# Kernel optimization log

Hardware: AMD Instinct MI355X
Metric: run time of the kernel (lower is better)

Reference implementation:

```python
import jax, jax.numpy as jnp
import numpy as np

B, S, D_IN, D_OUT, H = 4, 2048, 1024, 1024, 16
HD = D_OUT // H


def setup_inputs() -> dict:
    key = jax.random.key(0)
    ks = jax.random.split(key, 6)
    s_in = 1.0 / np.sqrt(D_IN)
    s_out = 1.0 / np.sqrt(D_OUT)
    return {
        "x": jax.random.normal(ks[0], (B, S, D_IN), dtype=jnp.float32),
        "W_q": jax.random.uniform(ks[1], (D_OUT, D_IN), jnp.float32, -s_in, s_in),
        "W_k": jax.random.uniform(ks[2], (D_OUT, D_IN), jnp.float32, -s_in, s_in),
        "W_v": jax.random.uniform(ks[3], (D_OUT, D_IN), jnp.float32, -s_in, s_in),
        "W_o": jax.random.uniform(ks[4], (D_OUT, D_OUT), jnp.float32, -s_out, s_out),
        "b_o": jax.random.uniform(ks[5], (D_OUT,), jnp.float32, -s_out, s_out),
    }


def reference(x, W_q, W_k, W_v, W_o, b_o):
    b, s, _ = x.shape
    # torch Linear: y = x @ W.T  (no qkv bias)
    q = (x @ W_q.T).reshape(b, s, H, HD).transpose(0, 2, 1, 3)  # [b,h,s,hd]
    k = (x @ W_k.T).reshape(b, s, H, HD).transpose(0, 2, 1, 3)
    v = (x @ W_v.T).reshape(b, s, H, HD).transpose(0, 2, 1, 3)
    scores = jnp.einsum("bhqd,bhkd->bhqk", q, k)  # [b,h,s,s]
    causal = jnp.triu(jnp.ones((s, s), dtype=bool), k=1)
    scores = jnp.where(causal, -jnp.inf, scores)
    attn = jax.nn.softmax(scores / np.sqrt(HD), axis=-1)
    # dropout p=0.0 -> identity
    ctx = jnp.einsum("bhqk,bhkd->bhqd", attn, v)  # [b,h,s,hd]
    ctx = ctx.transpose(0, 2, 1, 3).reshape(b, s, D_OUT)
    return ctx @ W_o.T + b_o
```

## Files before the change

### kernel.cpp

```cpp
#include <hip/hip_runtime.h>
#include <cstdint>
#include <cstddef>

#define S_LEN  2048
#define NHEAD  16
#define HDIM   64
#define KD     1024
#define BSROWS 8192

typedef __attribute__((ext_vector_type(4))) float          floatx4;
typedef __attribute__((ext_vector_type(8))) __bf16         bf16x8;
typedef __attribute__((ext_vector_type(8))) unsigned short ushort8v;
typedef __attribute__((ext_vector_type(4))) unsigned short ushort4v;
typedef __attribute__((ext_vector_type(4))) float          float4v;

__device__ __forceinline__ unsigned short f2bf(float f) {
  unsigned int u = __float_as_uint(f);
  u += 0x7fffu + ((u >> 16) & 1u);
  return (unsigned short)(u >> 16);
}

#if __has_builtin(__builtin_amdgcn_exp2f)
#define EXP2F(x) __builtin_amdgcn_exp2f(x)
#else
#define EXP2F(x) exp2f(x)
#endif

__device__ __forceinline__ unsigned int pack2bf(float a, float b) {
#if __has_builtin(__builtin_amdgcn_perm)
  return __builtin_amdgcn_perm(__float_as_uint(b), __float_as_uint(a), 0x07060302);
#else
  return (__float_as_uint(a) >> 16) | (__float_as_uint(b) & 0xffff0000u);
#endif
}

__device__ __forceinline__ void async_cp16(const void* gsrc, void* ldst) {
  __builtin_amdgcn_global_load_lds(
      (__attribute__((address_space(1))) void*)gsrc,
      (__attribute__((address_space(3))) void*)ldst,
      16, 0, 0);
}

#define XN4 2097152
#define WN4 262144

__global__ __launch_bounds__(256) void cvt_kernel(
    const float* __restrict__ x,  const float* __restrict__ wq,
    const float* __restrict__ wk, const float* __restrict__ wv,
    const float* __restrict__ wo,
    unsigned short* __restrict__ xb, unsigned short* __restrict__ wqkvb,
    unsigned short* __restrict__ wob)
{
  const int i = blockIdx.x * 256 + threadIdx.x;
  const float* src; unsigned short* dst; int off;
  if (i < XN4) { src = x; dst = xb; off = i; }
  else {
    const int j = i - XN4;
    if (j < WN4)          { src = wq; dst = wqkvb;           off = j; }
    else if (j < 2*WN4)   { src = wk; dst = wqkvb + 4*WN4;   off = j - WN4; }
    else if (j < 3*WN4)   { src = wv; dst = wqkvb + 8*WN4;   off = j - 2*WN4; }
    else                  { src = wo; dst = wob;             off = j - 3*WN4; }
  }
  const float4v v = ((const float4v*)src)[off];
  ushort4v o;
  o.x = f2bf(v.x); o.y = f2bf(v.y); o.z = f2bf(v.z); o.w = f2bf(v.w);
  ((ushort4v*)dst)[off] = o;
}

__global__ __launch_bounds__(256) void gemm_qkv(
    const unsigned short* __restrict__ A,
    const unsigned short* __restrict__ Bw,
    unsigned short* __restrict__ Qo,
    unsigned short* __restrict__ Ko,
    unsigned short* __restrict__ Vto)
{
  __shared__ unsigned short smem[17408];
  const int tid  = threadIdx.x;
  const int wave = tid >> 6, lane = tid & 63;
  const int quad = lane >> 4, l15 = lane & 15;
  const int wr = wave >> 1, wc = wave & 1;
  const int m0 = blockIdx.x * 128, n0 = blockIdx.y * 128;

  const int srow = lane >> 2;
  const int scol = ((lane & 3) ^ ((srow >> 1) & 3)) * 8;
  const unsigned short* gA = A  + (size_t)(m0 + wave * 32 + srow) * KD + scol;
  const unsigned short* gB = Bw + (size_t)(n0 + wave * 32 + srow) * KD + scol;

  const floatx4 fzero = {0.f, 0.f, 0.f, 0.f};
  floatx4 acc[4][4];
#pragma unroll
  for (int i = 0; i < 4; i++)
#pragma unroll
    for (int j = 0; j < 4; j++) acc[i][j] = fzero;

  {
    unsigned short* lA = smem + wave * 1024;
    unsigned short* lB = smem + 4096 + wave * 1024;
    async_cp16(gA,                    lA);
    async_cp16(gA + (size_t)16 * KD,  lA + 512);
    async_cp16(gB,                    lB);
    async_cp16(gB + (size_t)16 * KD,  lB + 512);
  }
  const int lsw = (l15 >> 1) & 3;

#pragma unroll 2
  for (int it = 0; it < 32; it++) {
    asm volatile("s_waitcnt vmcnt(0) lgkmcnt(0)\n\ts_barrier" ::: "memory");
    if (it + 1 < 32) {
      const int nb = (it + 1) & 1;
      const int ko = (it + 1) * 32;
      unsigned short* lA = smem + nb * 8192 + wave * 1024;
      unsigned short* lB = smem + nb * 8192 + 4096 + wave * 1024;
      async_cp16(gA + ko,                   lA);
      async_cp16(gA + ko + (size_t)16 * KD, lA + 512);
      async_cp16(gB + ko,                   lB);
      async_cp16(gB + ko + (size_t)16 * KD, lB + 512);
    }
    const unsigned short* As = smem + (it & 1) * 8192;
    const unsigned short* Bs = As + 4096;

    bf16x8 af[4], bfrag[4];
#pragma unroll
    for (int i = 0; i < 4; i++)
      af[i] = *(const bf16x8*)&As[(wr * 64 + i * 16 + l15) * 32 + (quad ^ lsw) * 8];
#pragma unroll
    for (int j = 0; j < 4; j++)
      bfrag[j] = *(const bf16x8*)&Bs[(wc * 64 + j * 16 + l15) * 32 + (quad ^ lsw) * 8];
#pragma unroll
    for (int i = 0; i < 4; i++)
#pragma unroll
      for (int j = 0; j < 4; j++)
        acc[i][j] = __builtin_amdgcn_mfma_f32_16x16x32_bf16(af[i], bfrag[j], acc[i][j], 0, 0, 0);
  }

  const int which = n0 >> 10;
  const int h0 = (n0 & 1023) >> 6;
  const int b = m0 >> 11, sl = m0 & 2047;

  if (which < 2) {
    unsigned short* dst = which ? Ko : Qo;
    const float scale = which ? 1.0f : 0.18033688011112042f;
    __syncthreads();
    const int crow = wr * 64 + quad * 4;
    const int ccol = wc * 64 + l15;
#pragma unroll
    for (int i = 0; i < 4; i++)
#pragma unroll
      for (int j = 0; j < 4; j++)
#pragma unroll
        for (int r = 0; r < 4; r++)
          smem[(crow + i * 16 + r) * 130 + ccol + j * 16] = f2bf(acc[i][j][r] * scale);
    __syncthreads();
#pragma unroll
    for (int t = 0; t < 8; t++) {
      const int c   = t * 256 + tid;
      const int hd8 = (c & 7) * 8;
      const int hh  = (c >> 3) & 1;
      const int s   = c >> 4;
      const ushort8v val = *(const ushort8v*)&smem[s * 130 + hh * 64 + hd8];
      *(ushort8v*)&dst[((size_t)((b * NHEAD + h0 + hh) * S_LEN + sl + s)) * HDIM + hd8] = val;
    }
  } else {
    __syncthreads();
    const int crow = wr * 64 + quad * 4;
    const int ccol = wc * 64 + l15;
#pragma unroll
    for (int i = 0; i < 4; i++)
#pragma unroll
      for (int j = 0; j < 4; j++) {
        ushort4v t4;
#pragma unroll
        for (int r = 0; r < 4; r++) t4[r] = f2bf(acc[i][j][r]);
        *(ushort4v*)&smem[(ccol + j * 16) * 136 + crow + i * 16] = t4;
      }
    __syncthreads();
#pragma unroll
    for (int t = 0; t < 8; t++) {
      const int c  = t * 256 + tid;
      const int nl = c >> 4, sc = (c & 15) * 8;
      const ushort8v val = *(const ushort8v*)&smem[nl * 136 + sc];
      *(ushort8v*)&Vto[((size_t)((b * NHEAD + h0 + (nl >> 6)) * HDIM + (nl & 63))) * S_LEN + sl + sc] = val;
    }
  }
}

__global__ __launch_bounds__(512, 4) void attn_kernel(
    const unsigned short* __restrict__ Qg_,
    const unsigned short* __restrict__ Kg_,
    const unsigned short* __restrict__ Vtg_,
    unsigned short* __restrict__ CTX)
{
  __shared__ unsigned short smem[33792];
  const int tid  = threadIdx.x, wave = tid >> 6, lane = tid & 63;
  const int quad = lane >> 4, l15 = lane & 15;
  unsigned short* Pw = smem + 16384 + wave * 2176;

  const int bh = (int)blockIdx.x;
  const int yy = (int)blockIdx.y;
  const int qt = (yy < 4) ? yy : (11 - yy);
  const int q0 = qt * 256;
  const size_t base = (size_t)bh * (S_LEN * HDIM);
  const unsigned short* Qg  = Qg_  + base;
  const unsigned short* Kg  = Kg_  + base;
  const unsigned short* Vtg = Vtg_ + base;
  const int qw = q0 + wave * 32;

  const int strow = lane >> 3;
  const int stxc  = (lane & 7) ^ strow;
  const unsigned short* kstage = Kg  + (size_t)(wave * 8 + strow) * HDIM  + stxc * 8;
  const unsigned short* vstage = Vtg + (size_t)(wave * 8 + strow) * S_LEN + stxc * 8;
  unsigned short* kd0 = smem + wave * 512;
  unsigned short* vd0 = smem + 4096 + wave * 512;

  async_cp16(kstage, kd0);
  async_cp16(vstage, vd0);

  bf16x8 qf[2][2];
#pragma unroll
  for (int qtile = 0; qtile < 2; qtile++)
#pragma unroll
    for (int ks = 0; ks < 2; ks++)
      qf[qtile][ks] = *(const bf16x8*)&Qg[(size_t)(qw + qtile * 16 + l15) * HDIM + ks * 32 + quad * 8];

  const int sw0 = ((quad)     ^ (l15 & 7)) * 8;
  const int sw1 = ((4 + quad) ^ (l15 & 7)) * 8;

  const floatx4 fzero = {0.f, 0.f, 0.f, 0.f};
  floatx4 O[2][4];
  float l_part[2] = {0.f, 0.f};
#pragma unroll
  for (int qtile = 0; qtile < 2; qtile++)
#pragma unroll
    for (int mt = 0; mt < 4; mt++) O[qtile][mt] = fzero;

  const int ntiles = 4 * (qt + 1);

  for (int j = 0; j < ntiles; j++) {
    asm volatile("s_waitcnt vmcnt(0) lgkmcnt(0)\n\ts_barrier" ::: "memory");
    if (j + 1 < ntiles) {
      const int nb = (j + 1) & 1;
      async_cp16(kstage + (size_t)(j + 1) * 64 * HDIM, kd0 + nb * 8192);
      async_cp16(vstage + (size_t)(j + 1) * 64,        vd0 + nb * 8192);
    }
    const int k0 = j * 64;
    if (k0 > qw + 31) continue;
    const unsigned short* Ksb = smem + (j & 1) * 8192;
    const unsigned short* Vsb = Ksb + 4096;
    const int krel = qw + 31 - k0;

    bf16x8 kf[4][2];
#pragma unroll
    for (int kt = 0; kt < 4; kt++) {
      if (kt * 16 <= krel) {
        const unsigned short* kr = &Ksb[(kt * 16 + l15) * 64];
        kf[kt][0] = *(const bf16x8*)(kr + sw0);
        kf[kt][1] = *(const bf16x8*)(kr + sw1);
      }
    }

#pragma unroll
    for (int qtile = 0; qtile < 2; qtile++) {
      const int kmax = qw + qtile * 16 + 15;
      if (k0 > kmax) continue;
      floatx4 sa[4];
#pragma unroll
      for (int kt = 0; kt < 4; kt++) sa[kt] = fzero;
#pragma unroll
      for (int kt = 0; kt < 4; kt++) {
        if (k0 + kt * 16 <= kmax) {
          sa[kt] = __builtin_amdgcn_mfma_f32_16x16x32_bf16(kf[kt][0], qf[qtile][0], sa[kt], 0, 0, 0);
          sa[kt] = __builtin_amdgcn_mfma_f32_16x16x32_bf16(kf[kt][1], qf[qtile][1], sa[kt], 0, 0, 0);
        }
      }
      const int qrow = qw + qtile * 16 + l15;
#pragma unroll
      for (int kt = 0; kt < 4; kt++) {
        const int kbase = k0 + kt * 16;
        unsigned short* pdst = &Pw[(qtile * 16 + l15) * 68 + kt * 16 + quad * 4];
        if (kbase <= kmax) {
          if (kbase + 15 > qw + qtile * 16) {
#pragma unroll
            for (int r = 0; r < 4; r++)
              if (kbase + quad * 4 + r > qrow) sa[kt][r] = -INFINITY;
          }
          const float p0 = EXP2F(sa[kt][0]), p1 = EXP2F(sa[kt][1]);
          const float p2 = EXP2F(sa[kt][2]), p3 = EXP2F(sa[kt][3]);
          l_part[qtile] += (p0 + p1) + (p2 + p3);
          uint2 pk; pk.x = pack2bf(p0, p1); pk.y = pack2bf(p2, p3);
          *(uint2*)pdst = pk;
        } else if (k0 + (kt >> 1) * 32 <= kmax) {
          uint2 z; z.x = 0u; z.y = 0u;
          *(uint2*)pdst = z;
        }
      }
    }
    asm volatile("s_waitcnt lgkmcnt(0)" ::: "memory");

#pragma unroll
    for (int ks = 0; ks < 2; ks++) {
      if (ks * 32 > krel) break;
      bf16x8 vf[4];
#pragma unroll
      for (int mt = 0; mt < 4; mt++)
        vf[mt] = *(const bf16x8*)(&Vsb[(mt * 16 + l15) * 64] + (ks ? sw1 : sw0));
#pragma unroll
      for (int qtile = 0; qtile < 2; qtile++) {
        if (k0 + ks * 32 > qw + qtile * 16 + 15) continue;
        const unsigned short* ps = &Pw[(qtile * 16 + l15) * 68 + ks * 32 + quad * 8];
        union { ushort4v h[2]; bf16x8 v; } pu;
        pu.h[0] = *(const ushort4v*)ps;
        pu.h[1] = *(const ushort4v*)(ps + 4);
#pragma unroll
        for (int mt = 0; mt < 4; mt++)
          O[qtile][mt] = __builtin_amdgcn_mfma_f32_16x16x32_bf16(vf[mt], pu.v, O[qtile][mt], 0, 0, 0);
      }
    }
  }

#pragma unroll
  for (int d = 16; d < 64; d <<= 1) {
    l_part[0] += __shfl_xor(l_part[0], d, 64);
    l_part[1] += __shfl_xor(l_part[1], d, 64);
  }

#pragma unroll
  for (int qtile = 0; qtile < 2; qtile++) {
    const float inv = 1.0f / l_part[qtile];
#pragma unroll
    for (int mt = 0; mt < 4; mt++)
#pragma unroll
      for (int a = 0; a < 2; a++) {
        const unsigned int pk =
            (unsigned int)f2bf(O[qtile][mt][2 * a] * inv) |
            ((unsigned int)f2bf(O[qtile][mt][2 * a + 1] * inv) << 16);
        *(unsigned int*)&Pw[(qtile * 16 + l15) * 68 + mt * 16 + quad * 4 + 2 * a] = pk;
      }
  }
  asm volatile("s_waitcnt lgkmcnt(0)" ::: "memory");
  const int b = bh >> 4, h = bh & 15;
#pragma unroll
  for (int it = 0; it < 4; it++) {
    const int g = it * 64 + lane;
    const int row = g >> 3, c8 = (g & 7) * 8;
    union { ushort4v h[2]; ushort8v v; } ou;
    ou.h[0] = *(const ushort4v*)&Pw[row * 68 + c8];
    ou.h[1] = *(const ushort4v*)&Pw[row * 68 + c8 + 4];
    const int s = qw + row;
    *(ushort8v*)&CTX[((size_t)(b * S_LEN + s)) * KD + h * HDIM + c8] = ou.v;
  }
}

__global__ __launch_bounds__(256) void gemm_out(
    const unsigned short* __restrict__ A,
    const unsigned short* __restrict__ Bw,
    const float* __restrict__ bias,
    float* __restrict__ out)
{
  __shared__ unsigned short smem[16384];
  const int tid  = threadIdx.x;
  const int wave = tid >> 6, lane = tid & 63;
  const int quad = lane >> 4, l15 = lane & 15;
  const int wr = wave >> 1, wc = wave & 1;
  const int m0 = blockIdx.x * 128, n0 = blockIdx.y * 128;

  const int srow = lane >> 2;
  const int scol = ((lane & 3) ^ ((srow >> 1) & 3)) * 8;
  const unsigned short* gA = A  + (size_t)(m0 + wave * 32 + srow) * KD + scol;
  const unsigned short* gB = Bw + (size_t)(n0 + wave * 32 + srow) * KD + scol;

  const floatx4 fzero = {0.f, 0.f, 0.f, 0.f};
  floatx4 acc[4][4];
#pragma unroll
  for (int i = 0; i < 4; i++)
#pragma unroll
    for (int j = 0; j < 4; j++) acc[i][j] = fzero;

  {
    unsigned short* lA = smem + wave * 1024;
    unsigned short* lB = smem + 4096 + wave * 1024;
    async_cp16(gA,                    lA);
    async_cp16(gA + (size_t)16 * KD,  lA + 512);
    async_cp16(gB,                    lB);
    async_cp16(gB + (size_t)16 * KD,  lB + 512);
  }
  const int lsw = (l15 >> 1) & 3;

#pragma unroll 2
  for (int it = 0; it < 32; it++) {
    asm volatile("s_waitcnt vmcnt(0) lgkmcnt(0)\n\ts_barrier" ::: "memory");
    if (it + 1 < 32) {
      const int nb = (it + 1) & 1;
      const int ko = (it + 1) * 32;
      unsigned short* lA = smem + nb * 8192 + wave * 1024;
      unsigned short* lB = smem + nb * 8192 + 4096 + wave * 1024;
      async_cp16(gA + ko,                   lA);
      async_cp16(gA + ko + (size_t)16 * KD, lA + 512);
      async_cp16(gB + ko,                   lB);
      async_cp16(gB + ko + (size_t)16 * KD, lB + 512);
    }
    const unsigned short* As = smem + (it & 1) * 8192;
    const unsigned short* Bs = As + 4096;

    bf16x8 af[4], bfrag[4];
#pragma unroll
    for (int i = 0; i < 4; i++)
      af[i] = *(const bf16x8*)&As[(wr * 64 + i * 16 + l15) * 32 + (quad ^ lsw) * 8];
#pragma unroll
    for (int j = 0; j < 4; j++)
      bfrag[j] = *(const bf16x8*)&Bs[(wc * 64 + j * 16 + l15) * 32 + (quad ^ lsw) * 8];
#pragma unroll
    for (int i = 0; i < 4; i++)
#pragma unroll
      for (int j = 0; j < 4; j++)
        acc[i][j] = __builtin_amdgcn_mfma_f32_16x16x32_bf16(af[i], bfrag[j], acc[i][j], 0, 0, 0);
  }

#pragma unroll
  for (int j = 0; j < 4; j++) {
    const int n = n0 + wc * 64 + j * 16 + l15;
    const float bb = bias[n];
#pragma unroll
    for (int i = 0; i < 4; i++) {
#pragma unroll
      for (int r = 0; r < 4; r++) {
        const int m = m0 + wr * 64 + i * 16 + quad * 4 + r;
        out[(size_t)m * KD + n] = acc[i][j][r] + bb;
      }
    }
  }
}

extern "C" void kernel_launch(void* const* d_in, const int* in_sizes, int n_in,
                              void* d_out, int out_size, void* d_ws, size_t ws_size,
                              hipStream_t stream) {
  (void)in_sizes; (void)n_in; (void)out_size;
  const float* x  = (const float*)d_in[0];
  const float* wq = (const float*)d_in[1];
  const float* wk = (const float*)d_in[2];
  const float* wv = (const float*)d_in[3];
  const float* wo = (const float*)d_in[4];
  const float* bo = (const float*)d_in[5];
  float* out = (float*)d_out;

  if (ws_size < (size_t)92274688) return;
  char* ws = (char*)d_ws;
  unsigned short* xb    = (unsigned short*)(ws);
  unsigned short* wqkvb = (unsigned short*)(ws + (size_t)16777216);
  unsigned short* wob   = (unsigned short*)(ws + (size_t)23068672);
  unsigned short* qws   = (unsigned short*)(ws + (size_t)25165824);
  unsigned short* kws   = (unsigned short*)(ws + (size_t)41943040);
  unsigned short* vtws  = (unsigned short*)(ws + (size_t)58720256);
  unsigned short* ctxws = (unsigned short*)(ws + (size_t)75497472);

  cvt_kernel<<<12288, 256, 0, stream>>>(x, wq, wk, wv, wo, xb, wqkvb, wob);
  gemm_qkv<<<dim3(64, 24), 256, 0, stream>>>(xb, wqkvb, qws, kws, vtws);
  attn_kernel<<<dim3(64, 8), 512, 0, stream>>>(qws, kws, vtws, ctxws);
  gemm_out<<<dim3(64, 8), 256, 0, stream>>>(ctxws, wob, bo, out);
}
```

Baseline: 252.8 us.

## Triple-buffer async global-to-LDS loads in GEMMs and attention, swizzle P scratch

```diff
diff --git a/kernel.cpp b/kernel.cpp
--- a/kernel.cpp
+++ b/kernel.cpp
@@ -74,7 +74,7 @@
     unsigned short* __restrict__ Ko,
     unsigned short* __restrict__ Vto)
 {
-  __shared__ unsigned short smem[17408];
+  __shared__ unsigned short smem[24576];
   const int tid  = threadIdx.x;
   const int wave = tid >> 6, lane = tid & 63;
   const int quad = lane >> 4, l15 = lane & 15;
@@ -85,6 +85,8 @@
   const int scol = ((lane & 3) ^ ((srow >> 1) & 3)) * 8;
   const unsigned short* gA = A  + (size_t)(m0 + wave * 32 + srow) * KD + scol;
   const unsigned short* gB = Bw + (size_t)(n0 + wave * 32 + srow) * KD + scol;
+  unsigned short* lA0 = smem + wave * 1024;
+  unsigned short* lB0 = smem + 4096 + wave * 1024;
 
   const floatx4 fzero = {0.f, 0.f, 0.f, 0.f};
   floatx4 acc[4][4];
@@ -93,32 +95,18 @@
 #pragma unroll
     for (int j = 0; j < 4; j++) acc[i][j] = fzero;
 
-  {
-    unsigned short* lA = smem + wave * 1024;
-    unsigned short* lB = smem + 4096 + wave * 1024;
-    async_cp16(gA,                    lA);
-    async_cp16(gA + (size_t)16 * KD,  lA + 512);
-    async_cp16(gB,                    lB);
-    async_cp16(gB + (size_t)16 * KD,  lB + 512);
+#pragma unroll
+  for (int t = 0; t < 2; t++) {
+    async_cp16(gA + t * 32,                   lA0 + t * 8192);
+    async_cp16(gA + t * 32 + (size_t)16 * KD, lA0 + t * 8192 + 512);
+    async_cp16(gB + t * 32,                   lB0 + t * 8192);
+    async_cp16(gB + t * 32 + (size_t)16 * KD, lB0 + t * 8192 + 512);
   }
   const int lsw = (l15 >> 1) & 3;
 
-#pragma unroll 2
-  for (int it = 0; it < 32; it++) {
-    asm volatile("s_waitcnt vmcnt(0) lgkmcnt(0)\n\ts_barrier" ::: "memory");
-    if (it + 1 < 32) {
-      const int nb = (it + 1) & 1;
-      const int ko = (it + 1) * 32;
-      unsigned short* lA = smem + nb * 8192 + wave * 1024;
-      unsigned short* lB = smem + nb * 8192 + 4096 + wave * 1024;
-      async_cp16(gA + ko,                   lA);
-      async_cp16(gA + ko + (size_t)16 * KD, lA + 512);
-      async_cp16(gB + ko,                   lB);
-      async_cp16(gB + ko + (size_t)16 * KD, lB + 512);
-    }
-    const unsigned short* As = smem + (it & 1) * 8192;
+  auto compute = [&](int it) {
+    const unsigned short* As = smem + (it % 3) * 8192;
     const unsigned short* Bs = As + 4096;
-
     bf16x8 af[4], bfrag[4];
 #pragma unroll
     for (int i = 0; i < 4; i++)
@@ -131,7 +119,22 @@
 #pragma unroll
       for (int j = 0; j < 4; j++)
         acc[i][j] = __builtin_amdgcn_mfma_f32_16x16x32_bf16(af[i], bfrag[j], acc[i][j], 0, 0, 0);
-  }
+  };
+
+  for (int it = 0; it < 31; it++) {
+    asm volatile("s_waitcnt vmcnt(4) lgkmcnt(0)\n\ts_barrier" ::: "memory");
+    if (it + 2 < 32) {
+      const int nb = (it + 2) % 3;
+      const int ko = (it + 2) * 32;
+      async_cp16(gA + ko,                   lA0 + nb * 8192);
+      async_cp16(gA + ko + (size_t)16 * KD, lA0 + nb * 8192 + 512);
+      async_cp16(gB + ko,                   lB0 + nb * 8192);
+      async_cp16(gB + ko + (size_t)16 * KD, lB0 + nb * 8192 + 512);
+    }
+    compute(it);
+  }
+  asm volatile("s_waitcnt vmcnt(0) lgkmcnt(0)\n\ts_barrier" ::: "memory");
+  compute(31);
 
   const int which = n0 >> 10;
   const int h0 = (n0 & 1023) >> 6;
@@ -190,10 +193,11 @@
     const unsigned short* __restrict__ Vtg_,
     unsigned short* __restrict__ CTX)
 {
-  __shared__ unsigned short smem[33792];
+  __shared__ unsigned short smem[40960];
   const int tid  = threadIdx.x, wave = tid >> 6, lane = tid & 63;
   const int quad = lane >> 4, l15 = lane & 15;
-  unsigned short* Pw = smem + 16384 + wave * 2176;
+  unsigned short* Pw = smem + 24576 + wave * 2048;
+  const int swp = l15 & 7;
 
   const int bh = (int)blockIdx.x;
   const int yy = (int)blockIdx.y;
@@ -212,8 +216,12 @@
   unsigned short* kd0 = smem + wave * 512;
   unsigned short* vd0 = smem + 4096 + wave * 512;
 
+  const int ntiles = 4 * (qt + 1);
+
   async_cp16(kstage, kd0);
   async_cp16(vstage, vd0);
+  async_cp16(kstage + (size_t)64 * HDIM, kd0 + 8192);
+  async_cp16(vstage + 64,                vd0 + 8192);
 
   bf16x8 qf[2][2];
 #pragma unroll
@@ -233,18 +241,10 @@
 #pragma unroll
     for (int mt = 0; mt < 4; mt++) O[qtile][mt] = fzero;
 
-  const int ntiles = 4 * (qt + 1);
-
-  for (int j = 0; j < ntiles; j++) {
-    asm volatile("s_waitcnt vmcnt(0) lgkmcnt(0)\n\ts_barrier" ::: "memory");
-    if (j + 1 < ntiles) {
-      const int nb = (j + 1) & 1;
-      async_cp16(kstage + (size_t)(j + 1) * 64 * HDIM, kd0 + nb * 8192);
-      async_cp16(vstage + (size_t)(j + 1) * 64,        vd0 + nb * 8192);
-    }
+  auto tile = [&](int j) {
     const int k0 = j * 64;
-    if (k0 > qw + 31) continue;
-    const unsigned short* Ksb = smem + (j & 1) * 8192;
+    if (k0 > qw + 31) return;
+    const unsigned short* Ksb = smem + (j % 3) * 8192;
     const unsigned short* Vsb = Ksb + 4096;
     const int krel = qw + 31 - k0;
 
@@ -276,7 +276,8 @@
 #pragma unroll
       for (int kt = 0; kt < 4; kt++) {
         const int kbase = k0 + kt * 16;
-        unsigned short* pdst = &Pw[(qtile * 16 + l15) * 68 + kt * 16 + quad * 4];
+        unsigned short* pdst = &Pw[(qtile * 16 + l15) * 64 +
+                                   ((kt * 2 + (quad >> 1)) ^ swp) * 8 + (quad & 1) * 4];
         if (kbase <= kmax) {
           if (kbase + 15 > qw + qtile * 16) {
 #pragma unroll
@@ -306,16 +307,26 @@
 #pragma unroll
       for (int qtile = 0; qtile < 2; qtile++) {
         if (k0 + ks * 32 > qw + qtile * 16 + 15) continue;
-        const unsigned short* ps = &Pw[(qtile * 16 + l15) * 68 + ks * 32 + quad * 8];
-        union { ushort4v h[2]; bf16x8 v; } pu;
-        pu.h[0] = *(const ushort4v*)ps;
-        pu.h[1] = *(const ushort4v*)(ps + 4);
+        const bf16x8 pv = *(const bf16x8*)&Pw[(qtile * 16 + l15) * 64 +
+                                              ((ks * 4 + quad) ^ swp) * 8];
 #pragma unroll
         for (int mt = 0; mt < 4; mt++)
-          O[qtile][mt] = __builtin_amdgcn_mfma_f32_16x16x32_bf16(vf[mt], pu.v, O[qtile][mt], 0, 0, 0);
-      }
-    }
-  }
+          O[qtile][mt] = __builtin_amdgcn_mfma_f32_16x16x32_bf16(vf[mt], pv, O[qtile][mt], 0, 0, 0);
+      }
+    }
+  };
+
+  for (int j = 0; j < ntiles - 1; j++) {
+    asm volatile("s_waitcnt vmcnt(2) lgkmcnt(0)\n\ts_barrier" ::: "memory");
+    if (j + 2 < ntiles) {
+      const int nb = (j + 2) % 3;
+      async_cp16(kstage + (size_t)(j + 2) * 64 * HDIM, kd0 + nb * 8192);
+      async_cp16(vstage + (size_t)(j + 2) * 64,        vd0 + nb * 8192);
+    }
+    tile(j);
+  }
+  asm volatile("s_waitcnt vmcnt(0) lgkmcnt(0)\n\ts_barrier" ::: "memory");
+  tile(ntiles - 1);
 
 #pragma unroll
   for (int d = 16; d < 64; d <<= 1) {
@@ -333,7 +344,8 @@
         const unsigned int pk =
             (unsigned int)f2bf(O[qtile][mt][2 * a] * inv) |
             ((unsigned int)f2bf(O[qtile][mt][2 * a + 1] * inv) << 16);
-        *(unsigned int*)&Pw[(qtile * 16 + l15) * 68 + mt * 16 + quad * 4 + 2 * a] = pk;
+        *(unsigned int*)&Pw[(qtile * 16 + l15) * 64 +
+                            ((mt * 2 + (quad >> 1)) ^ swp) * 8 + (quad & 1) * 4 + 2 * a] = pk;
       }
   }
   asm volatile("s_waitcnt lgkmcnt(0)" ::: "memory");
@@ -341,12 +353,10 @@
 #pragma unroll
   for (int it = 0; it < 4; it++) {
     const int g = it * 64 + lane;
-    const int row = g >> 3, c8 = (g & 7) * 8;
-    union { ushort4v h[2]; ushort8v v; } ou;
-    ou.h[0] = *(const ushort4v*)&Pw[row * 68 + c8];
-    ou.h[1] = *(const ushort4v*)&Pw[row * 68 + c8 + 4];
+    const int row = g >> 3, lc = g & 7;
+    const ushort8v ov = *(const ushort8v*)&Pw[row * 64 + (lc ^ (row & 7)) * 8];
     const int s = qw + row;
-    *(ushort8v*)&CTX[((size_t)(b * S_LEN + s)) * KD + h * HDIM + c8] = ou.v;
+    *(ushort8v*)&CTX[((size_t)(b * S_LEN + s)) * KD + h * HDIM + lc * 8] = ov;
   }
 }
 
@@ -356,7 +366,7 @@
     const float* __restrict__ bias,
     float* __restrict__ out)
 {
-  __shared__ unsigned short smem[16384];
+  __shared__ unsigned short smem[24576];
   const int tid  = threadIdx.x;
   const int wave = tid >> 6, lane = tid & 63;
   const int quad = lane >> 4, l15 = lane & 15;
@@ -367,6 +377,8 @@
   const int scol = ((lane & 3) ^ ((srow >> 1) & 3)) * 8;
   const unsigned short* gA = A  + (size_t)(m0 + wave * 32 + srow) * KD + scol;
   const unsigned short* gB = Bw + (size_t)(n0 + wave * 32 + srow) * KD + scol;
+  unsigned short* lA0 = smem + wave * 1024;
+  unsigned short* lB0 = smem + 4096 + wave * 1024;
 
   const floatx4 fzero = {0.f, 0.f, 0.f, 0.f};
   floatx4 acc[4][4];
@@ -375,32 +387,18 @@
 #pragma unroll
     for (int j = 0; j < 4; j++) acc[i][j] = fzero;
 
-  {
-    unsigned short* lA = smem + wave * 1024;
-    unsigned short* lB = smem + 4096 + wave * 1024;
-    async_cp16(gA,                    lA);
-    async_cp16(gA + (size_t)16 * KD,  lA + 512);
-    async_cp16(gB,                    lB);
-    async_cp16(gB + (size_t)16 * KD,  lB + 512);
+#pragma unroll
+  for (int t = 0; t < 2; t++) {
+    async_cp16(gA + t * 32,                   lA0 + t * 8192);
+    async_cp16(gA + t * 32 + (size_t)16 * KD, lA0 + t * 8192 + 512);
+    async_cp16(gB + t * 32,                   lB0 + t * 8192);
+    async_cp16(gB + t * 32 + (size_t)16 * KD, lB0 + t * 8192 + 512);
   }
   const int lsw = (l15 >> 1) & 3;
 
-#pragma unroll 2
-  for (int it = 0; it < 32; it++) {
-    asm volatile("s_waitcnt vmcnt(0) lgkmcnt(0)\n\ts_barrier" ::: "memory");
-    if (it + 1 < 32) {
-      const int nb = (it + 1) & 1;
-      const int ko = (it + 1) * 32;
-      unsigned short* lA = smem + nb * 8192 + wave * 1024;
-      unsigned short* lB = smem + nb * 8192 + 4096 + wave * 1024;
-      async_cp16(gA + ko,                   lA);
-      async_cp16(gA + ko + (size_t)16 * KD, lA + 512);
-      async_cp16(gB + ko,                   lB);
-      async_cp16(gB + ko + (size_t)16 * KD, lB + 512);
-    }
-    const unsigned short* As = smem + (it & 1) * 8192;
+  auto compute = [&](int it) {
+    const unsigned short* As = smem + (it % 3) * 8192;
     const unsigned short* Bs = As + 4096;
-
     bf16x8 af[4], bfrag[4];
 #pragma unroll
     for (int i = 0; i < 4; i++)
@@ -413,7 +411,22 @@
 #pragma unroll
       for (int j = 0; j < 4; j++)
         acc[i][j] = __builtin_amdgcn_mfma_f32_16x16x32_bf16(af[i], bfrag[j], acc[i][j], 0, 0, 0);
-  }
+  };
+
+  for (int it = 0; it < 31; it++) {
+    asm volatile("s_waitcnt vmcnt(4) lgkmcnt(0)\n\ts_barrier" ::: "memory");
+    if (it + 2 < 32) {
+      const int nb = (it + 2) % 3;
+      const int ko = (it + 2) * 32;
+      async_cp16(gA + ko,                   lA0 + nb * 8192);
+      async_cp16(gA + ko + (size_t)16 * KD, lA0 + nb * 8192 + 512);
+      async_cp16(gB + ko,                   lB0 + nb * 8192);
+      async_cp16(gB + ko + (size_t)16 * KD, lB0 + nb * 8192 + 512);
+    }
+    compute(it);
+  }
+  asm volatile("s_waitcnt vmcnt(0) lgkmcnt(0)\n\ts_barrier" ::: "memory");
+  compute(31);
 
 #pragma unroll
   for (int j = 0; j < 4; j++) {
```

Result: slower. 258.5 us (+2.3%).

## Halve attention query tile to 128 rows, one 16-row tile per wave

Applied to the files above, without the earlier changes.

```diff
diff --git a/kernel.cpp b/kernel.cpp
--- a/kernel.cpp
+++ b/kernel.cpp
@@ -184,26 +184,26 @@
   }
 }
 
-__global__ __launch_bounds__(512, 4) void attn_kernel(
+__global__ __launch_bounds__(512, 6) void attn_kernel(
     const unsigned short* __restrict__ Qg_,
     const unsigned short* __restrict__ Kg_,
     const unsigned short* __restrict__ Vtg_,
     unsigned short* __restrict__ CTX)
 {
-  __shared__ unsigned short smem[33792];
+  __shared__ unsigned short smem[25088];
   const int tid  = threadIdx.x, wave = tid >> 6, lane = tid & 63;
   const int quad = lane >> 4, l15 = lane & 15;
-  unsigned short* Pw = smem + 16384 + wave * 2176;
+  unsigned short* Pw = smem + 16384 + wave * 1088;
 
   const int bh = (int)blockIdx.x;
   const int yy = (int)blockIdx.y;
-  const int qt = (yy < 4) ? yy : (11 - yy);
-  const int q0 = qt * 256;
+  const int qt = (yy < 4) ? yy : (yy < 8) ? (11 - yy) : (yy < 12) ? yy : (27 - yy);
+  const int q0 = qt * 128;
   const size_t base = (size_t)bh * (S_LEN * HDIM);
   const unsigned short* Qg  = Qg_  + base;
   const unsigned short* Kg  = Kg_  + base;
   const unsigned short* Vtg = Vtg_ + base;
-  const int qw = q0 + wave * 32;
+  const int qw = q0 + wave * 16;
 
   const int strow = lane >> 3;
   const int stxc  = (lane & 7) ^ strow;
@@ -215,25 +215,21 @@
   async_cp16(kstage, kd0);
   async_cp16(vstage, vd0);
 
-  bf16x8 qf[2][2];
-#pragma unroll
-  for (int qtile = 0; qtile < 2; qtile++)
-#pragma unroll
-    for (int ks = 0; ks < 2; ks++)
-      qf[qtile][ks] = *(const bf16x8*)&Qg[(size_t)(qw + qtile * 16 + l15) * HDIM + ks * 32 + quad * 8];
+  bf16x8 qf[2];
+#pragma unroll
+  for (int ks = 0; ks < 2; ks++)
+    qf[ks] = *(const bf16x8*)&Qg[(size_t)(qw + l15) * HDIM + ks * 32 + quad * 8];
 
   const int sw0 = ((quad)     ^ (l15 & 7)) * 8;
   const int sw1 = ((4 + quad) ^ (l15 & 7)) * 8;
 
   const floatx4 fzero = {0.f, 0.f, 0.f, 0.f};
-  floatx4 O[2][4];
-  float l_part[2] = {0.f, 0.f};
-#pragma unroll
-  for (int qtile = 0; qtile < 2; qtile++)
-#pragma unroll
-    for (int mt = 0; mt < 4; mt++) O[qtile][mt] = fzero;
-
-  const int ntiles = 4 * (qt + 1);
+  floatx4 O[4];
+  float l_part = 0.f;
+#pragma unroll
+  for (int mt = 0; mt < 4; mt++) O[mt] = fzero;
+
+  const int ntiles = 2 * qt + 2;
 
   for (int j = 0; j < ntiles; j++) {
     asm volatile("s_waitcnt vmcnt(0) lgkmcnt(0)\n\ts_barrier" ::: "memory");
@@ -243,55 +239,42 @@
       async_cp16(vstage + (size_t)(j + 1) * 64,        vd0 + nb * 8192);
     }
     const int k0 = j * 64;
-    if (k0 > qw + 31) continue;
+    if (k0 > qw + 15) continue;
     const unsigned short* Ksb = smem + (j & 1) * 8192;
     const unsigned short* Vsb = Ksb + 4096;
-    const int krel = qw + 31 - k0;
-
-    bf16x8 kf[4][2];
+    const int krel = qw + 15 - k0;
+
+    floatx4 sa[4];
+#pragma unroll
+    for (int kt = 0; kt < 4; kt++) sa[kt] = fzero;
 #pragma unroll
     for (int kt = 0; kt < 4; kt++) {
       if (kt * 16 <= krel) {
         const unsigned short* kr = &Ksb[(kt * 16 + l15) * 64];
-        kf[kt][0] = *(const bf16x8*)(kr + sw0);
-        kf[kt][1] = *(const bf16x8*)(kr + sw1);
-      }
-    }
-
-#pragma unroll
-    for (int qtile = 0; qtile < 2; qtile++) {
-      const int kmax = qw + qtile * 16 + 15;
-      if (k0 > kmax) continue;
-      floatx4 sa[4];
-#pragma unroll
-      for (int kt = 0; kt < 4; kt++) sa[kt] = fzero;
-#pragma unroll
-      for (int kt = 0; kt < 4; kt++) {
-        if (k0 + kt * 16 <= kmax) {
-          sa[kt] = __builtin_amdgcn_mfma_f32_16x16x32_bf16(kf[kt][0], qf[qtile][0], sa[kt], 0, 0, 0);
-          sa[kt] = __builtin_amdgcn_mfma_f32_16x16x32_bf16(kf[kt][1], qf[qtile][1], sa[kt], 0, 0, 0);
+        sa[kt] = __builtin_amdgcn_mfma_f32_16x16x32_bf16(*(const bf16x8*)(kr + sw0), qf[0], sa[kt], 0, 0, 0);
+        sa[kt] = __builtin_amdgcn_mfma_f32_16x16x32_bf16(*(const bf16x8*)(kr + sw1), qf[1], sa[kt], 0, 0, 0);
+      }
+    }
+
+    const int qrow = qw + l15;
+#pragma unroll
+    for (int kt = 0; kt < 4; kt++) {
+      const int kbase = k0 + kt * 16;
+      unsigned short* pdst = &Pw[l15 * 68 + kt * 16 + quad * 4];
+      if (kt * 16 <= krel) {
+        if (kbase + 15 > qw) {
+#pragma unroll
+          for (int r = 0; r < 4; r++)
+            if (kbase + quad * 4 + r > qrow) sa[kt][r] = -INFINITY;
         }
-      }
-      const int qrow = qw + qtile * 16 + l15;
-#pragma unroll
-      for (int kt = 0; kt < 4; kt++) {
-        const int kbase = k0 + kt * 16;
-        unsigned short* pdst = &Pw[(qtile * 16 + l15) * 68 + kt * 16 + quad * 4];
-        if (kbase <= kmax) {
-          if (kbase + 15 > qw + qtile * 16) {
-#pragma unroll
-            for (int r = 0; r < 4; r++)
-              if (kbase + quad * 4 + r > qrow) sa[kt][r] = -INFINITY;
-          }
-          const float p0 = EXP2F(sa[kt][0]), p1 = EXP2F(sa[kt][1]);
-          const float p2 = EXP2F(sa[kt][2]), p3 = EXP2F(sa[kt][3]);
-          l_part[qtile] += (p0 + p1) + (p2 + p3);
-          uint2 pk; pk.x = pack2bf(p0, p1); pk.y = pack2bf(p2, p3);
-          *(uint2*)pdst = pk;
-        } else if (k0 + (kt >> 1) * 32 <= kmax) {
-          uint2 z; z.x = 0u; z.y = 0u;
-          *(uint2*)pdst = z;
-        }
+        const float p0 = EXP2F(sa[kt][0]), p1 = EXP2F(sa[kt][1]);
+        const float p2 = EXP2F(sa[kt][2]), p3 = EXP2F(sa[kt][3]);
+        l_part += (p0 + p1) + (p2 + p3);
+        uint2 pk; pk.x = pack2bf(p0, p1); pk.y = pack2bf(p2, p3);
+        *(uint2*)pdst = pk;
+      } else if ((kt >> 1) * 32 <= krel) {
+        uint2 z; z.x = 0u; z.y = 0u;
+        *(uint2*)pdst = z;
       }
     }
     asm volatile("s_waitcnt lgkmcnt(0)" ::: "memory");
@@ -299,47 +282,38 @@
 #pragma unroll
     for (int ks = 0; ks < 2; ks++) {
       if (ks * 32 > krel) break;
-      bf16x8 vf[4];
-#pragma unroll
-      for (int mt = 0; mt < 4; mt++)
-        vf[mt] = *(const bf16x8*)(&Vsb[(mt * 16 + l15) * 64] + (ks ? sw1 : sw0));
-#pragma unroll
-      for (int qtile = 0; qtile < 2; qtile++) {
-        if (k0 + ks * 32 > qw + qtile * 16 + 15) continue;
-        const unsigned short* ps = &Pw[(qtile * 16 + l15) * 68 + ks * 32 + quad * 8];
-        union { ushort4v h[2]; bf16x8 v; } pu;
-        pu.h[0] = *(const ushort4v*)ps;
-        pu.h[1] = *(const ushort4v*)(ps + 4);
-#pragma unroll
-        for (int mt = 0; mt < 4; mt++)
-          O[qtile][mt] = __builtin_amdgcn_mfma_f32_16x16x32_bf16(vf[mt], pu.v, O[qtile][mt], 0, 0, 0);
-      }
-    }
-  }
-
-#pragma unroll
-  for (int d = 16; d < 64; d <<= 1) {
-    l_part[0] += __shfl_xor(l_part[0], d, 64);
-    l_part[1] += __shfl_xor(l_part[1], d, 64);
-  }
-
-#pragma unroll
-  for (int qtile = 0; qtile < 2; qtile++) {
-    const float inv = 1.0f / l_part[qtile];
+      const unsigned short* ps = &Pw[l15 * 68 + ks * 32 + quad * 8];
+      union { ushort4v h[2]; bf16x8 v; } pu;
+      pu.h[0] = *(const ushort4v*)ps;
+      pu.h[1] = *(const ushort4v*)(ps + 4);
+#pragma unroll
+      for (int mt = 0; mt < 4; mt++) {
+        const bf16x8 vf = *(const bf16x8*)(&Vsb[(mt * 16 + l15) * 64] + (ks ? sw1 : sw0));
+        O[mt] = __builtin_amdgcn_mfma_f32_16x16x32_bf16(vf, pu.v, O[mt], 0, 0, 0);
+      }
+    }
+  }
+
+#pragma unroll
+  for (int d = 16; d < 64; d <<= 1)
+    l_part += __shfl_xor(l_part, d, 64);
+
+  {
+    const float inv = 1.0f / l_part;
 #pragma unroll
     for (int mt = 0; mt < 4; mt++)
 #pragma unroll
       for (int a = 0; a < 2; a++) {
         const unsigned int pk =
-            (unsigned int)f2bf(O[qtile][mt][2 * a] * inv) |
-            ((unsigned int)f2bf(O[qtile][mt][2 * a + 1] * inv) << 16);
-        *(unsigned int*)&Pw[(qtile * 16 + l15) * 68 + mt * 16 + quad * 4 + 2 * a] = pk;
+            (unsigned int)f2bf(O[mt][2 * a] * inv) |
+            ((unsigned int)f2bf(O[mt][2 * a + 1] * inv) << 16);
+        *(unsigned int*)&Pw[l15 * 68 + mt * 16 + quad * 4 + 2 * a] = pk;
       }
   }
   asm volatile("s_waitcnt lgkmcnt(0)" ::: "memory");
   const int b = bh >> 4, h = bh & 15;
 #pragma unroll
-  for (int it = 0; it < 4; it++) {
+  for (int it = 0; it < 2; it++) {
     const int g = it * 64 + lane;
     const int row = g >> 3, c8 = (g & 7) * 8;
     union { ushort4v h[2]; ushort8v v; } ou;
@@ -454,6 +428,6 @@
 
   cvt_kernel<<<12288, 256, 0, stream>>>(x, wq, wk, wv, wo, xb, wqkvb, wob);
   gemm_qkv<<<dim3(64, 24), 256, 0, stream>>>(xb, wqkvb, qws, kws, vtws);
-  attn_kernel<<<dim3(64, 8), 512, 0, stream>>>(qws, kws, vtws, ctxws);
+  attn_kernel<<<dim3(64, 16), 512, 0, stream>>>(qws, kws, vtws, ctxws);
   gemm_out<<<dim3(64, 8), 256, 0, stream>>>(ctxws, wob, bo, out);
 }
```

Result: faster. 242.3 us (-4.1%).
